# Kernel tuning notes

Measured on AMD Instinct MI355X. Metric: run time of the kernel, lower is better.

The kernel has to match this reference:

```python
import jax, jax.numpy as jnp
import numpy as np

B, N = 4096, 8192
RETURN_W, SHARPE_W, CONC_W, CONF_W, BENT_W, AUX_W = 1.0, 0.1, 0.01, 0.1, 0.01, 0.1
RETURN_TEMP = 20.0
NEG = -1e30
EPS = 1e-8


def setup_inputs() -> dict:
    key = jax.random.key(0)
    ks = jax.random.split(key, 6)
    portfolio_returns = jax.random.normal(ks[0], (B,), dtype=jnp.float32) * 0.01
    weights = jax.random.uniform(ks[1], (B, N), dtype=jnp.float32)
    confidence = jax.random.uniform(ks[2], (B, N), dtype=jnp.float32)
    actual_returns = jax.random.normal(ks[3], (B, N), dtype=jnp.float32) * 0.02
    masks = (jax.random.uniform(ks[4], (B, N)) > 0.1).astype(jnp.float32)
    scores = jax.random.normal(ks[5], (B, N), dtype=jnp.float32)
    return {
        "portfolio_returns": portfolio_returns,
        "weights": weights,
        "confidence": confidence,
        "actual_returns": actual_returns,
        "masks": masks,
        "scores": scores,
    }


def _ranking_loss(scores, returns, masks):
    # Vectorized ListNet loss: masked softmax over valid stocks per sample.
    valid = masks > 0  # (B, N) bool
    n_valid = valid.sum(axis=-1)  # (B,)
    target = jax.nn.softmax(jnp.where(valid, returns * RETURN_TEMP, NEG), axis=-1)
    log_dist = jax.nn.log_softmax(jnp.where(valid, scores, NEG), axis=-1)
    per_sample = -(target * jnp.where(valid, log_dist, 0.0)).sum(axis=-1)
    per_sample = per_sample / jnp.maximum(n_valid, 1).astype(per_sample.dtype)
    sample_ok = n_valid >= 2  # (B,) samples with >=2 valid stocks
    num_ok = sample_ok.sum()
    total = jnp.where(sample_ok, per_sample, 0.0).sum()
    return jnp.where(num_ok > 0, total / jnp.maximum(num_ok, 1), 0.0)


def reference(portfolio_returns, weights, confidence, actual_returns, masks, scores):
    # return maximization
    mean_return = portfolio_returns.mean()
    return_loss = -mean_return
    # sharpe (batch_size > 1; torch .std() uses ddof=1)
    return_std = jnp.std(portfolio_returns, ddof=1)
    sharpe_loss = jnp.clip(-mean_return / (return_std + 0.01), -10.0, 10.0)
    # concentration (weight entropy)
    concentration_loss = -(weights * jnp.log(weights + EPS)).sum(axis=-1).mean()
    # confidence loss
    selected_conf = (weights * confidence * masks).sum(axis=-1)
    total_weight = (weights * masks).sum(axis=-1) + EPS
    per_sample_conf = selected_conf / total_weight
    conf_targets = jax.nn.sigmoid(portfolio_returns * 50.0)
    confidence_loss = jnp.mean((per_sample_conf - conf_targets) ** 2)
    # batch entropy (stocks never valid contribute exactly 0, so no index-filter needed)
    normalized_weights = weights / (weights.sum(axis=-1, keepdims=True) + EPS)
    avg_sel = (normalized_weights * masks).mean(axis=0)  # (N,)
    avg_sel = avg_sel / (avg_sel.sum() + EPS)
    batch_entropy = -(avg_sel * jnp.log(avg_sel + EPS)).sum()
    batch_entropy_loss = -batch_entropy
    # auxiliary ranking loss
    auxiliary_loss = _ranking_loss(scores, actual_returns, masks)
    total_loss = (
        RETURN_W * return_loss
        + SHARPE_W * sharpe_loss
        + CONC_W * concentration_loss
        + CONF_W * confidence_loss
        + BENT_W * batch_entropy_loss
        + AUX_W * auxiliary_loss
    )
    return total_loss
```

## Files before the change

### kernel.cpp

```cpp
#include <hip/hip_runtime.h>
#include <math.h>

#define BB 4096
#define NN 8192
#define EPSF 1e-8f

typedef float f32x4 __attribute__((ext_vector_type(4)));

#define SCAL 4096
#define CS   8192
#define PP   16384

__global__ void init_ws(float* __restrict__ ws) {
    int i = blockIdx.x * blockDim.x + threadIdx.x;
    if (i < 12288) ws[SCAL + i] = 0.f;
}

__global__ __launch_bounds__(256) void rowsum_k(const float* __restrict__ w,
                                                float* __restrict__ ws) {
    const int wave = threadIdx.x >> 6, lane = threadIdx.x & 63;
    const int row = blockIdx.x * 4 + wave;
    const f32x4* w4 = (const f32x4*)(w + (size_t)row * NN);
    float s = 0.f;
#pragma unroll
    for (int c = 0; c < 32; ++c) {
        f32x4 v = w4[c * 64 + lane];
        s += (v.x + v.y) + (v.z + v.w);
    }
#pragma unroll
    for (int off = 32; off; off >>= 1) s += __shfl_xor(s, off);
    if (lane == 0) ws[row] = 1.f / (s + EPSF);
}

template<int ROWS, int MODE>
__global__ __launch_bounds__(512) void main_k(
    const float* __restrict__ pr, const float* __restrict__ w,
    const float* __restrict__ cf, const float* __restrict__ ar,
    const float* __restrict__ mk, const float* __restrict__ sc,
    float* ws)
{
    const int t = threadIdx.x;
    const int wave = t >> 6, lane = t & 63;
    const int rowBase = blockIdx.x * ROWS;

    __shared__ float part[ROWS][8][8];

    float csum[16];
#pragma unroll
    for (int j = 0; j < 16; ++j) csum[j] = 0.f;

    for (int rr = 0; rr < ROWS; ++rr) {
        const int row = rowBase + rr;
        const size_t base = (size_t)row * NN;
        const float inv = ws[row];
        const f32x4* w4 = (const f32x4*)(w + base);
        const f32x4* c4 = (const f32x4*)(cf + base);
        const f32x4* a4 = (const f32x4*)(ar + base);
        const f32x4* m4 = (const f32x4*)(mk + base);
        const f32x4* s4 = (const f32x4*)(sc + base);

        float conc = 0.f, scf = 0.f, tw = 0.f, nv = 0.f;
        float Zr = 0.f, A = 0.f, Zs = 0.f;
#define PROC(WK, MKV, CK, RK, SK, IDX) {                          \
        const float wk = (WK), mval = (MKV);                      \
        conc = fmaf(wk, __logf(wk + EPSF), conc);                 \
        const float wmk = wk * mval;                              \
        tw += wmk; scf = fmaf(wmk, (CK), scf);                    \
        nv += mval;                                               \
        const float er = __expf((RK) * 20.f) * mval;              \
        Zr += er; A = fmaf(er, (SK), A);                          \
        Zs = fmaf(__expf((SK)), mval, Zs);                        \
        csum[IDX] = fmaf(wmk, inv, csum[IDX]); }

#pragma unroll
        for (int j = 0; j < 4; ++j) {
            const int f4 = t + j * 512;
            f32x4 wv = w4[f4];
            f32x4 mv = __builtin_nontemporal_load(m4 + f4);
            f32x4 cv = __builtin_nontemporal_load(c4 + f4);
            f32x4 rv = __builtin_nontemporal_load(a4 + f4);
            f32x4 sv = __builtin_nontemporal_load(s4 + f4);
            PROC(wv.x, mv.x, cv.x, rv.x, sv.x, j * 4 + 0)
            PROC(wv.y, mv.y, cv.y, rv.y, sv.y, j * 4 + 1)
            PROC(wv.z, mv.z, cv.z, rv.z, sv.z, j * 4 + 2)
            PROC(wv.w, mv.w, cv.w, rv.w, sv.w, j * 4 + 3)
        }
#undef PROC

#pragma unroll
        for (int off = 32; off; off >>= 1) {
            conc += __shfl_xor(conc, off);
            scf  += __shfl_xor(scf, off);
            tw   += __shfl_xor(tw, off);
            nv   += __shfl_xor(nv, off);
            Zr   += __shfl_xor(Zr, off);
            A    += __shfl_xor(A, off);
            Zs   += __shfl_xor(Zs, off);
        }
        if (lane == 0) {
            float* p = part[rr][wave];
            p[0] = conc; p[1] = scf; p[2] = tw; p[3] = nv;
            p[4] = Zr;   p[5] = A;   p[6] = Zs;
        }
    }
    __syncthreads();

    float c0 = 0.f, c1 = 0.f, c2 = 0.f, c3 = 0.f;
    if (t < ROWS) {
        float CO = 0, SC = 0, TW = 0, NV = 0, ZR = 0, AA = 0, ZS = 0;
        for (int k = 0; k < 8; ++k) {
            float* p = part[t][k];
            CO += p[0]; SC += p[1]; TW += p[2]; NV += p[3];
            ZR += p[4]; AA += p[5]; ZS += p[6];
        }
        c0 = CO;
        const float psc = SC / (TW + EPSF);
        const float ct = 1.f / (1.f + __expf(-50.f * pr[rowBase + t]));
        const float d = psc - ct;
        c1 = d * d;
        if (NV >= 2.f) {
            c2 = (__logf(ZS) - AA / ZR) / NV;
            c3 = 1.f;
        }
    }
    if (wave == 0) {
#pragma unroll
        for (int off = 32; off; off >>= 1) {
            c0 += __shfl_xor(c0, off);
            c1 += __shfl_xor(c1, off);
            c2 += __shfl_xor(c2, off);
            c3 += __shfl_xor(c3, off);
        }
        if (lane == 0) {
            atomicAdd(&ws[SCAL + 0], c0);
            atomicAdd(&ws[SCAL + 1], c1);
            atomicAdd(&ws[SCAL + 2], c2);
            atomicAdd(&ws[SCAL + 3], c3);
        }
    }

    if (MODE == 0) {
#pragma unroll
        for (int j = 0; j < 4; ++j) {
            const int f4 = t + j * 512;
            atomicAdd(&ws[CS + 4 * f4 + 0], csum[j * 4 + 0]);
            atomicAdd(&ws[CS + 4 * f4 + 1], csum[j * 4 + 1]);
            atomicAdd(&ws[CS + 4 * f4 + 2], csum[j * 4 + 2]);
            atomicAdd(&ws[CS + 4 * f4 + 3], csum[j * 4 + 3]);
        }
    } else {
        f32x4* dst = (f32x4*)(ws + PP) + (size_t)blockIdx.x * (NN / 4);
#pragma unroll
        for (int j = 0; j < 4; ++j) {
            const int f4 = t + j * 512;
            f32x4 v;
            v.x = csum[j * 4 + 0]; v.y = csum[j * 4 + 1];
            v.z = csum[j * 4 + 2]; v.w = csum[j * 4 + 3];
            __builtin_nontemporal_store(v, dst + f4);
        }
    }
}

__global__ __launch_bounds__(256) void colreduce_k(const float* __restrict__ src,
                                                   float* __restrict__ ws) {
    const int c = blockIdx.x * 256 + threadIdx.x;
    const int k0 = blockIdx.y * 128;
    float s = 0.f;
    for (int k = 0; k < 128; ++k) s += src[(size_t)(k0 + k) * NN + c];
    atomicAdd(&ws[CS + c], s);
}

__device__ __forceinline__ float block_sum_1024(float v) {
    __shared__ float scm[16];
#pragma unroll
    for (int off = 32; off; off >>= 1) v += __shfl_xor(v, off);
    if ((threadIdx.x & 63) == 0) scm[threadIdx.x >> 6] = v;
    __syncthreads();
    if (threadIdx.x == 0) {
        float a = 0.f;
        for (int k = 0; k < 16; ++k) a += scm[k];
        scm[0] = a;
    }
    __syncthreads();
    float r = scm[0];
    __syncthreads();
    return r;
}

__global__ __launch_bounds__(1024) void finalize(
    const float* __restrict__ pr, const float* __restrict__ ws,
    float* __restrict__ out)
{
    const int t = threadIdx.x;

    float s = 0.f, ssq = 0.f;
    for (int i = t; i < BB; i += 1024) { float v = pr[i]; s += v; ssq = fmaf(v, v, ssq); }
    float Tc = 0.f;
    for (int i = t; i < NN; i += 1024) Tc += ws[CS + i];

    float S  = block_sum_1024(s);
    float SS = block_sum_1024(ssq);
    float T  = block_sum_1024(Tc);

    const float mean = S / (float)BB;
    const float denom = T / (float)BB + EPSF;

    float ent = 0.f;
    for (int i = t; i < NN; i += 1024) {
        float a = ws[CS + i] / (float)BB;
        float na = a / denom;
        ent = fmaf(na, __logf(na + EPSF), ent);
    }
    float ENT = block_sum_1024(ent);

    if (t == 0) {
        float var = (SS - (float)BB * mean * mean) / (float)(BB - 1);
        float sd = sqrtf(fmaxf(var, 0.f));
        float sharpe = -mean / (sd + 0.01f);
        sharpe = fminf(fmaxf(sharpe, -10.f), 10.f);
        float conc_loss = -ws[SCAL + 0] / (float)BB;
        float conf_loss =  ws[SCAL + 1] / (float)BB;
        float nok = ws[SCAL + 3];
        float aux = (nok > 0.f) ? ws[SCAL + 2] / fmaxf(nok, 1.f) : 0.f;
        out[0] = 1.0f * (-mean)
               + 0.1f * sharpe
               + 0.01f * conc_loss
               + 0.1f * conf_loss
               + 0.01f * ENT
               + 0.1f * aux;
    }
}

extern "C" void kernel_launch(void* const* d_in, const int* in_sizes, int n_in,
                              void* d_out, int out_size, void* d_ws, size_t ws_size,
                              hipStream_t stream) {
    const float* pr = (const float*)d_in[0];
    const float* w  = (const float*)d_in[1];
    const float* cf = (const float*)d_in[2];
    const float* ar = (const float*)d_in[3];
    const float* mk = (const float*)d_in[4];
    const float* sc = (const float*)d_in[5];
    float* ws = (float*)d_ws;
    float* out = (float*)d_out;

    const size_t needBytes = ((size_t)PP + (size_t)1024 * NN) * sizeof(float);
    const bool partial = (ws_size >= needBytes);

    init_ws<<<48, 256, 0, stream>>>(ws);
    rowsum_k<<<1024, 256, 0, stream>>>(w, ws);
    if (partial) {
        main_k<4, 1><<<1024, 512, 0, stream>>>(pr, w, cf, ar, mk, sc, ws);
        colreduce_k<<<dim3(32, 8), 256, 0, stream>>>(ws + PP, ws);
    } else {
        main_k<8, 0><<<512, 512, 0, stream>>>(pr, w, cf, ar, mk, sc, ws);
    }
    finalize<<<1, 1024, 0, stream>>>(pr, ws, out);
}
```

Baseline: 169.2 us.

## Fuse row-sum pass into main kernel by holding weight rows in registers

Removes the separate rowsum kernel. Each main-kernel block now loads its four weight rows into registers, reduces them to inverse row sums through shared memory, and then reuses those registers in the main accumulation pass. This avoids reading the weight matrix from memory a second time and drops one launch. In exchange it needs 64 extra VGPRs for the held weights under a launch bound of 512 threads with a minimum of 4 blocks, adds a block-wide barrier before the streaming loads of the other four inputs begin, and moves the per-row scalar reduction after the column-sum store.

```diff
diff --git a/kernel.cpp b/kernel.cpp
--- a/kernel.cpp
+++ b/kernel.cpp
@@ -16,24 +16,8 @@
     if (i < 12288) ws[SCAL + i] = 0.f;
 }
 
-__global__ __launch_bounds__(256) void rowsum_k(const float* __restrict__ w,
-                                                float* __restrict__ ws) {
-    const int wave = threadIdx.x >> 6, lane = threadIdx.x & 63;
-    const int row = blockIdx.x * 4 + wave;
-    const f32x4* w4 = (const f32x4*)(w + (size_t)row * NN);
-    float s = 0.f;
-#pragma unroll
-    for (int c = 0; c < 32; ++c) {
-        f32x4 v = w4[c * 64 + lane];
-        s += (v.x + v.y) + (v.z + v.w);
-    }
-#pragma unroll
-    for (int off = 32; off; off >>= 1) s += __shfl_xor(s, off);
-    if (lane == 0) ws[row] = 1.f / (s + EPSF);
-}
-
-template<int ROWS, int MODE>
-__global__ __launch_bounds__(512) void main_k(
+template<int MODE>
+__global__ __launch_bounds__(512, 4) void main_k(
     const float* __restrict__ pr, const float* __restrict__ w,
     const float* __restrict__ cf, const float* __restrict__ ar,
     const float* __restrict__ mk, const float* __restrict__ sc,
@@ -41,26 +25,68 @@
 {
     const int t = threadIdx.x;
     const int wave = t >> 6, lane = t & 63;
-    const int rowBase = blockIdx.x * ROWS;
-
-    __shared__ float part[ROWS][8][8];
+    const int rowBase = blockIdx.x * 4;
+
+    __shared__ float rpark[8][4];
+    __shared__ float park[4][8][8];
+
+    const size_t rbase = (size_t)rowBase * (NN / 4);
+    const f32x4* w4 = (const f32x4*)w;
+    const f32x4* m4 = (const f32x4*)mk;
+    const f32x4* c4 = (const f32x4*)cf;
+    const f32x4* a4 = (const f32x4*)ar;
+    const f32x4* s4 = (const f32x4*)sc;
+
+    f32x4 wreg[16];
+#pragma unroll
+    for (int rr = 0; rr < 4; ++rr)
+#pragma unroll
+        for (int j = 0; j < 4; ++j)
+            wreg[rr * 4 + j] = __builtin_nontemporal_load(
+                w4 + rbase + (size_t)rr * (NN / 4) + t + j * 512);
+
+    float rs0, rs1, rs2, rs3;
+    {
+        f32x4 a, b, c, d;
+        a = wreg[0];  b = wreg[1];  c = wreg[2];  d = wreg[3];
+        rs0 = ((a.x + a.y) + (a.z + a.w)) + ((b.x + b.y) + (b.z + b.w))
+            + ((c.x + c.y) + (c.z + c.w)) + ((d.x + d.y) + (d.z + d.w));
+        a = wreg[4];  b = wreg[5];  c = wreg[6];  d = wreg[7];
+        rs1 = ((a.x + a.y) + (a.z + a.w)) + ((b.x + b.y) + (b.z + b.w))
+            + ((c.x + c.y) + (c.z + c.w)) + ((d.x + d.y) + (d.z + d.w));
+        a = wreg[8];  b = wreg[9];  c = wreg[10]; d = wreg[11];
+        rs2 = ((a.x + a.y) + (a.z + a.w)) + ((b.x + b.y) + (b.z + b.w))
+            + ((c.x + c.y) + (c.z + c.w)) + ((d.x + d.y) + (d.z + d.w));
+        a = wreg[12]; b = wreg[13]; c = wreg[14]; d = wreg[15];
+        rs3 = ((a.x + a.y) + (a.z + a.w)) + ((b.x + b.y) + (b.z + b.w))
+            + ((c.x + c.y) + (c.z + c.w)) + ((d.x + d.y) + (d.z + d.w));
+    }
+#pragma unroll
+    for (int off = 32; off; off >>= 1) {
+        rs0 += __shfl_xor(rs0, off);
+        rs1 += __shfl_xor(rs1, off);
+        rs2 += __shfl_xor(rs2, off);
+        rs3 += __shfl_xor(rs3, off);
+    }
+    if (lane == 0) {
+        rpark[wave][0] = rs0; rpark[wave][1] = rs1;
+        rpark[wave][2] = rs2; rpark[wave][3] = rs3;
+    }
+    __syncthreads();
+
+    float inv[4];
+#pragma unroll
+    for (int r = 0; r < 4; ++r) {
+        float acc = 0.f;
+#pragma unroll
+        for (int k = 0; k < 8; ++k) acc += rpark[k][r];
+        inv[r] = 1.f / (acc + EPSF);
+    }
 
     float csum[16];
 #pragma unroll
     for (int j = 0; j < 16; ++j) csum[j] = 0.f;
 
-    for (int rr = 0; rr < ROWS; ++rr) {
-        const int row = rowBase + rr;
-        const size_t base = (size_t)row * NN;
-        const float inv = ws[row];
-        const f32x4* w4 = (const f32x4*)(w + base);
-        const f32x4* c4 = (const f32x4*)(cf + base);
-        const f32x4* a4 = (const f32x4*)(ar + base);
-        const f32x4* m4 = (const f32x4*)(mk + base);
-        const f32x4* s4 = (const f32x4*)(sc + base);
-
-        float conc = 0.f, scf = 0.f, tw = 0.f, nv = 0.f;
-        float Zr = 0.f, A = 0.f, Zs = 0.f;
 #define PROC(WK, MKV, CK, RK, SK, IDX) {                          \
         const float wk = (WK), mval = (MKV);                      \
         conc = fmaf(wk, __logf(wk + EPSF), conc);                 \
@@ -70,23 +96,26 @@
         const float er = __expf((RK) * 20.f) * mval;              \
         Zr += er; A = fmaf(er, (SK), A);                          \
         Zs = fmaf(__expf((SK)), mval, Zs);                        \
-        csum[IDX] = fmaf(wmk, inv, csum[IDX]); }
-
+        csum[IDX] = fmaf(wmk, invr, csum[IDX]); }
+
+#pragma unroll
+    for (int rr = 0; rr < 4; ++rr) {
+        const size_t base = rbase + (size_t)rr * (NN / 4) + t;
+        const float invr = inv[rr];
+        float conc = 0.f, scf = 0.f, tw = 0.f, nv = 0.f;
+        float Zr = 0.f, A = 0.f, Zs = 0.f;
 #pragma unroll
         for (int j = 0; j < 4; ++j) {
-            const int f4 = t + j * 512;
-            f32x4 wv = w4[f4];
-            f32x4 mv = __builtin_nontemporal_load(m4 + f4);
-            f32x4 cv = __builtin_nontemporal_load(c4 + f4);
-            f32x4 rv = __builtin_nontemporal_load(a4 + f4);
-            f32x4 sv = __builtin_nontemporal_load(s4 + f4);
+            const f32x4 wv = wreg[rr * 4 + j];
+            const f32x4 mv = __builtin_nontemporal_load(m4 + base + j * 512);
+            const f32x4 cv = __builtin_nontemporal_load(c4 + base + j * 512);
+            const f32x4 rv = __builtin_nontemporal_load(a4 + base + j * 512);
+            const f32x4 sv = __builtin_nontemporal_load(s4 + base + j * 512);
             PROC(wv.x, mv.x, cv.x, rv.x, sv.x, j * 4 + 0)
             PROC(wv.y, mv.y, cv.y, rv.y, sv.y, j * 4 + 1)
             PROC(wv.z, mv.z, cv.z, rv.z, sv.z, j * 4 + 2)
             PROC(wv.w, mv.w, cv.w, rv.w, sv.w, j * 4 + 3)
         }
-#undef PROC
-
 #pragma unroll
         for (int off = 32; off; off >>= 1) {
             conc += __shfl_xor(conc, off);
@@ -98,48 +127,23 @@
             Zs   += __shfl_xor(Zs, off);
         }
         if (lane == 0) {
-            float* p = part[rr][wave];
+            float* p = park[rr][wave];
             p[0] = conc; p[1] = scf; p[2] = tw; p[3] = nv;
             p[4] = Zr;   p[5] = A;   p[6] = Zs;
         }
     }
-    __syncthreads();
-
-    float c0 = 0.f, c1 = 0.f, c2 = 0.f, c3 = 0.f;
-    if (t < ROWS) {
-        float CO = 0, SC = 0, TW = 0, NV = 0, ZR = 0, AA = 0, ZS = 0;
-        for (int k = 0; k < 8; ++k) {
-            float* p = part[t][k];
-            CO += p[0]; SC += p[1]; TW += p[2]; NV += p[3];
-            ZR += p[4]; AA += p[5]; ZS += p[6];
-        }
-        c0 = CO;
-        const float psc = SC / (TW + EPSF);
-        const float ct = 1.f / (1.f + __expf(-50.f * pr[rowBase + t]));
-        const float d = psc - ct;
-        c1 = d * d;
-        if (NV >= 2.f) {
-            c2 = (__logf(ZS) - AA / ZR) / NV;
-            c3 = 1.f;
-        }
-    }
-    if (wave == 0) {
-#pragma unroll
-        for (int off = 32; off; off >>= 1) {
-            c0 += __shfl_xor(c0, off);
-            c1 += __shfl_xor(c1, off);
-            c2 += __shfl_xor(c2, off);
-            c3 += __shfl_xor(c3, off);
-        }
-        if (lane == 0) {
-            atomicAdd(&ws[SCAL + 0], c0);
-            atomicAdd(&ws[SCAL + 1], c1);
-            atomicAdd(&ws[SCAL + 2], c2);
-            atomicAdd(&ws[SCAL + 3], c3);
-        }
-    }
-
-    if (MODE == 0) {
+#undef PROC
+
+    if (MODE == 1) {
+        f32x4* dst = (f32x4*)(ws + PP) + (size_t)blockIdx.x * (NN / 4);
+#pragma unroll
+        for (int j = 0; j < 4; ++j) {
+            f32x4 v;
+            v.x = csum[j * 4 + 0]; v.y = csum[j * 4 + 1];
+            v.z = csum[j * 4 + 2]; v.w = csum[j * 4 + 3];
+            __builtin_nontemporal_store(v, dst + t + j * 512);
+        }
+    } else {
 #pragma unroll
         for (int j = 0; j < 4; ++j) {
             const int f4 = t + j * 512;
@@ -148,15 +152,39 @@
             atomicAdd(&ws[CS + 4 * f4 + 2], csum[j * 4 + 2]);
             atomicAdd(&ws[CS + 4 * f4 + 3], csum[j * 4 + 3]);
         }
-    } else {
-        f32x4* dst = (f32x4*)(ws + PP) + (size_t)blockIdx.x * (NN / 4);
-#pragma unroll
-        for (int j = 0; j < 4; ++j) {
-            const int f4 = t + j * 512;
-            f32x4 v;
-            v.x = csum[j * 4 + 0]; v.y = csum[j * 4 + 1];
-            v.z = csum[j * 4 + 2]; v.w = csum[j * 4 + 3];
-            __builtin_nontemporal_store(v, dst + f4);
+    }
+
+    __syncthreads();
+
+    if (t < 64) {
+        float c0 = 0.f, c1 = 0.f, c2 = 0.f, c3 = 0.f;
+        if (lane < 4) {
+            float CO = 0, SC = 0, TW = 0, NV = 0, ZR = 0, AA = 0, ZS = 0;
+#pragma unroll
+            for (int k = 0; k < 8; ++k) {
+                const float* p = park[lane][k];
+                CO += p[0]; SC += p[1]; TW += p[2]; NV += p[3];
+                ZR += p[4]; AA += p[5]; ZS += p[6];
+            }
+            c0 = CO;
+            const float psc = SC / (TW + EPSF);
+            const float ct = 1.f / (1.f + __expf(-50.f * pr[rowBase + lane]));
+            const float d = psc - ct;
+            c1 = d * d;
+            if (NV >= 2.f) {
+                c2 = (__logf(ZS) - AA / ZR) / NV;
+                c3 = 1.f;
+            }
+        }
+        c0 += __shfl_xor(c0, 1); c0 += __shfl_xor(c0, 2);
+        c1 += __shfl_xor(c1, 1); c1 += __shfl_xor(c1, 2);
+        c2 += __shfl_xor(c2, 1); c2 += __shfl_xor(c2, 2);
+        c3 += __shfl_xor(c3, 1); c3 += __shfl_xor(c3, 2);
+        if (lane == 0) {
+            atomicAdd(&ws[SCAL + 0], c0);
+            atomicAdd(&ws[SCAL + 1], c1);
+            atomicAdd(&ws[SCAL + 2], c2);
+            atomicAdd(&ws[SCAL + 3], c3);
         }
     }
 }
@@ -247,12 +275,11 @@
     const bool partial = (ws_size >= needBytes);
 
     init_ws<<<48, 256, 0, stream>>>(ws);
-    rowsum_k<<<1024, 256, 0, stream>>>(w, ws);
     if (partial) {
-        main_k<4, 1><<<1024, 512, 0, stream>>>(pr, w, cf, ar, mk, sc, ws);
+        main_k<1><<<1024, 512, 0, stream>>>(pr, w, cf, ar, mk, sc, ws);
         colreduce_k<<<dim3(32, 8), 256, 0, stream>>>(ws + PP, ws);
     } else {
-        main_k<8, 0><<<512, 512, 0, stream>>>(pr, w, cf, ar, mk, sc, ws);
+        main_k<0><<<1024, 512, 0, stream>>>(pr, w, cf, ar, mk, sc, ws);
     }
     finalize<<<1, 1024, 0, stream>>>(pr, ws, out);
 }
```

New measurement: 205.3 us. +21.3%, slower.
